# Kernel optimization log

Hardware: AMD Instinct MI355X
Metric: run time of the kernel (lower is better)

The kernel has to match this reference:

```python
import jax, jax.numpy as jnp
import numpy as np

N, E = 25000, 400000
D_NODE, D_EDGE_IN, D_EH, D_H, D_DUAL = 128, 16, 128, 256, 128


def layer_norm(x, g, b, eps=1e-5):
    mu = jnp.mean(x, axis=-1, keepdims=True)
    var = jnp.mean((x - mu) ** 2, axis=-1, keepdims=True)
    return (x - mu) * jax.lax.rsqrt(var + eps) * g + b


def setup_inputs() -> dict:
    key = jax.random.key(0)
    ks = jax.random.split(key, 20)

    def w(k, shape):
        return (jax.random.normal(k, shape, dtype=jnp.float32) * 0.05)

    inp = {
        "node_embedding": jax.random.normal(ks[0], (N, D_NODE), dtype=jnp.float32),
        "edge_index": jax.random.randint(ks[1], (2, E), 0, N, dtype=jnp.int64),
        "edge_attr": jax.random.normal(ks[2], (E, D_EDGE_IN), dtype=jnp.float32),
        "dual_node_emb": jax.random.normal(ks[3], (E, D_DUAL), dtype=jnp.float32),
        "atom_reactivity_logits": jax.random.normal(ks[4], (N,), dtype=jnp.float32),
        "W_be1": w(ks[5], (D_EDGE_IN, D_EH)), "b_be1": jnp.zeros((D_EH,), jnp.float32),
        "g_be1": jnp.ones((D_EH,), jnp.float32), "bb_be1": jnp.zeros((D_EH,), jnp.float32),
        "W_be2": w(ks[6], (D_EH, D_EH)), "b_be2": jnp.zeros((D_EH,), jnp.float32),
        "g_be2": jnp.ones((D_EH,), jnp.float32), "bb_be2": jnp.zeros((D_EH,), jnp.float32),
        "W_be3": w(ks[7], (D_EH, D_EH)), "b_be3": jnp.zeros((D_EH,), jnp.float32),
        "g_be3": jnp.ones((D_EH,), jnp.float32), "bb_be3": jnp.zeros((D_EH,), jnp.float32),
        # DualGraphBondReactivityPredictor
        "W_d1": w(ks[8], (D_DUAL, D_H)), "b_d1": jnp.zeros((D_H,), jnp.float32),
        "W_d2": w(ks[9], (D_H, D_H)), "b_d2": jnp.zeros((D_H,), jnp.float32),
        "W_do": w(ks[10], (D_H, 1)), "b_do": jnp.zeros((1,), jnp.float32),
        # main head: in = 2*D_NODE + D_EH + 3 = 387
        "W_f1": w(ks[11], (2 * D_NODE + D_EH + 3, D_H)), "b_f1": jnp.zeros((D_H,), jnp.float32),
        "W_f2": w(ks[12], (D_H, D_H)), "b_f2": jnp.zeros((D_H,), jnp.float32),
        "W_bo": w(ks[13], (D_H, 1)), "b_bo": jnp.zeros((1,), jnp.float32),
    }
    return inp


def reference(node_embedding, edge_index, edge_attr, dual_node_emb, atom_reactivity_logits,
              W_be1, b_be1, g_be1, bb_be1, W_be2, b_be2, g_be2, bb_be2,
              W_be3, b_be3, g_be3, bb_be3,
              W_d1, b_d1, W_d2, b_d2, W_do, b_do,
              W_f1, b_f1, W_f2, b_f2, W_bo, b_bo):
    src, dst = edge_index[0], edge_index[1]

    # BondEmbedding (dropout = identity in eval mode)
    e = jax.nn.silu(layer_norm(edge_attr @ W_be1 + b_be1, g_be1, bb_be1))
    e = jax.nn.silu(layer_norm(e @ W_be2 + b_be2, g_be2, bb_be2))
    e = jax.nn.silu(layer_norm(e @ W_be3 + b_be3, g_be3, bb_be3))  # [E, D_EH]

    atom_p = jax.nn.sigmoid(atom_reactivity_logits)  # [N]
    p_src = atom_p[src][:, None]  # [E,1]
    p_dst = atom_p[dst][:, None]

    # dual-graph bond reactivity
    d = jax.nn.silu(dual_node_emb @ W_d1 + b_d1)
    d = jax.nn.silu(d @ W_d2 + b_d2)
    dual_p = jax.nn.sigmoid((d @ W_do + b_do)[:, 0])[:, None]  # [E,1]

    feats = jnp.concatenate(
        [node_embedding[src], node_embedding[dst], e, dual_p, p_src, p_dst], axis=-1
    )  # [E, 2*D_NODE + D_EH + 3]

    x = jax.nn.silu(feats @ W_f1 + b_f1)
    x = jax.nn.silu(x @ W_f2 + b_f2)
    return (x @ W_bo + b_bo)[:, 0]  # [E]
```

## Files before the change

### kernel.cpp

```cpp
#include <hip/hip_runtime.h>
#include <hip/hip_bf16.h>
#include <stdint.h>

typedef __attribute__((ext_vector_type(8))) short bf16x8;
typedef __attribute__((ext_vector_type(4))) float f32x4;
typedef __attribute__((ext_vector_type(4))) float float4v;

__device__ __forceinline__ uint16_t bfc(float x){
    __hip_bfloat16 h = __float2bfloat16(x);
    return __builtin_bit_cast(uint16_t, h);
}
__device__ __forceinline__ uint32_t pk2(float a, float b){
    return (uint32_t)bfc(a) | ((uint32_t)bfc(b) << 16);
}
__device__ __forceinline__ float fsigmoid(float x){ return 1.0f / (1.0f + __expf(-x)); }
__device__ __forceinline__ float fsilu(float x){ return x * fsigmoid(x); }

__device__ __forceinline__ bf16x8 pack8(float4v lo, float4v hi){
    bf16x8 r;
    r[0]=(short)bfc(lo[0]); r[1]=(short)bfc(lo[1]);
    r[2]=(short)bfc(lo[2]); r[3]=(short)bfc(lo[3]);
    r[4]=(short)bfc(hi[0]); r[5]=(short)bfc(hi[1]);
    r[6]=(short)bfc(hi[2]); r[7]=(short)bfc(hi[3]);
    return r;
}

#define SZ_BE1 4096
#define SZ_128 16384
#define SZ_D1  32768
#define SZ_D2  65536
#define SZ_F1  98304
#define OFF_BE1 0
#define OFF_BE2 (OFF_BE1 + SZ_BE1)
#define OFF_BE3 (OFF_BE2 + SZ_128)
#define OFF_D1  (OFF_BE3 + SZ_128)
#define OFF_D2  (OFF_D1 + SZ_D1)
#define OFF_F1  (OFF_D2 + SZ_D2)
#define OFF_F2  (OFF_F1 + SZ_F1)
#define WS_ELEMS (OFF_F2 + SZ_D2)

__device__ __forceinline__ int fragpos(int k, int c, int OUT){
    int kt = k >> 5, ct = c >> 4;
    int fid = kt * (OUT >> 4) + ct;
    int ln = ((k & 31) >> 3) * 16 + (c & 15);
    return fid * 512 + ln * 8 + (k & 7);
}

__global__ void __launch_bounds__(256)
prep_w(const float* __restrict__ Wbe1, const float* __restrict__ Wbe2,
       const float* __restrict__ Wbe3, const float* __restrict__ Wd1,
       const float* __restrict__ Wd2,  const float* __restrict__ Wf1,
       const float* __restrict__ Wf2,  uint16_t* __restrict__ ws){
    int t = blockIdx.x * 256 + threadIdx.x;
    if (t >= WS_ELEMS) return;
    if (t < OFF_BE2) {
        int u = t;            int k = u >> 7, c = u & 127;
        float v = (k < 16) ? Wbe1[k * 128 + c] : 0.0f;
        ws[OFF_BE1 + fragpos(k, c, 128)] = bfc(v);
    } else if (t < OFF_BE3) {
        int u = t - OFF_BE2;  int k = u >> 7, c = u & 127;
        ws[OFF_BE2 + fragpos(k, c, 128)] = bfc(Wbe2[u]);
    } else if (t < OFF_D1) {
        int u = t - OFF_BE3;  int k = u >> 7, c = u & 127;
        ws[OFF_BE3 + fragpos(k, c, 128)] = bfc(Wbe3[u]);
    } else if (t < OFF_D2) {
        int u = t - OFF_D1;   int k = u >> 8, c = u & 255;
        ws[OFF_D1 + fragpos(k, c, 256)] = bfc(Wd1[u]);
    } else if (t < OFF_F1) {
        int u = t - OFF_D2;   int k = u >> 8, c = u & 255;
        ws[OFF_D2 + fragpos(k, c, 256)] = bfc(Wd2[u]);
    } else if (t < OFF_F2) {
        int u = t - OFF_F1;   int k = u >> 8, c = u & 255;
        ws[OFF_F1 + fragpos(k, c, 256)] = bfc(Wf1[u]);
    } else {
        int u = t - OFF_F2;   int k = u >> 8, c = u & 255;
        ws[OFF_F2 + fragpos(k, c, 256)] = bfc(Wf2[u]);
    }
}

__global__ void __launch_bounds__(256)
prep_n(const float* __restrict__ src, uint16_t* __restrict__ dst, int n){
    int t = blockIdx.x * 256 + threadIdx.x;
    if (t < n) dst[t] = bfc(src[t]);
}

typedef const __attribute__((address_space(1))) void gas_void;
typedef __attribute__((address_space(3))) void las_void;
__device__ __forceinline__ void g2l16(const void* g, void* l){
    __builtin_amdgcn_global_load_lds((gas_void*)g, (las_void*)l, 16, 0, 0);
}

#define LDS_TOTAL 135168

__global__ void __launch_bounds__(512) __attribute__((amdgpu_waves_per_eu(2, 2)))
bond_fast_kernel(const int* __restrict__ edge_index,
                 const float* __restrict__ edge_attr, const float* __restrict__ dual_emb,
                 const float* __restrict__ logits,
                 const float* __restrict__ b_be1, const float* __restrict__ g_be1, const float* __restrict__ bb_be1,
                 const float* __restrict__ b_be2, const float* __restrict__ g_be2, const float* __restrict__ bb_be2,
                 const float* __restrict__ b_be3, const float* __restrict__ g_be3, const float* __restrict__ bb_be3,
                 const float* __restrict__ b_d1, const float* __restrict__ b_d2,
                 const float* __restrict__ W_do, const float* __restrict__ b_do,
                 const float* __restrict__ W_f1, const float* __restrict__ b_f1,
                 const float* __restrict__ b_f2,
                 const float* __restrict__ W_bo, const float* __restrict__ b_bo,
                 const uint16_t* __restrict__ ws, float* __restrict__ out, int E)
{
    __shared__ char lds[LDS_TOTAL];
    const int t    = threadIdx.x;
    const int wave = t >> 6;
    const int lane = t & 63;
    const int li   = lane & 15, lg = lane >> 4;
    const int eg   = wave >> 1;
    const int ch   = wave & 1;
    const int e0b  = blockIdx.x * 128;

    char* bufE = lds;
    char* h256 = lds + 32768;
    uint16_t* wb0 = (uint16_t*)(lds + 98304);
    uint16_t* wb1 = (uint16_t*)(lds + 114688);
    float* ps  = (float*)(lds + 131072);
    float* pd  = (float*)(lds + 131584);
    int* sidx  = (int*)(lds + 132096);
    int* didx  = (int*)(lds + 132608);
    float* dpp = (float*)(lds + 133120);
    float* bop = (float*)(lds + 134144);

    const uint8_t*  wsb = (const uint8_t*)ws;
    const uint16_t* nbf = ws + WS_ELEMS;

    if (t < 128) {
        int e = e0b + t; if (e >= E) e = E - 1;
        int s_ = edge_index[e];
        int d_ = edge_index[E + e];
        sidx[t] = s_; didx[t] = d_;
        ps[t] = fsigmoid(logits[s_]);
        pd[t] = fsigmoid(logits[d_]);
    }

    int cur = 0;
    auto stageW = [&](int elemoff, int big){
        uint8_t* dst = (uint8_t*)(cur ? wb0 : wb1) + t * 16;
        const uint8_t* g = wsb + (size_t)elemoff * 2 + t * 16;
        g2l16(g, dst);
        if (big) g2l16(g + 8192, dst + 8192);
    };
    auto stepend = [&](){ __syncthreads(); cur ^= 1; };
    auto curbuf  = [&]() -> const uint16_t* { return cur ? wb1 : wb0; };

    f32x4 acc[2][8];

    auto ldf = [&](const uint16_t* w, int fid) -> bf16x8 {
        return *(const bf16x8*)(w + fid * 512 + lane * 8);
    };
    auto grpBE = [&](const uint16_t* w, bf16x8 a0){
        #pragma unroll
        for (int ct = 0; ct < 8; ++ct){
            bf16x8 b = ldf(w, ct);
            acc[0][ct] = __builtin_amdgcn_mfma_f32_16x16x32_bf16(a0, b, acc[0][ct], 0, 0, 0);
        }
    };
    auto grp256 = [&](const uint16_t* w, bf16x8 a0, bf16x8 a1){
        #pragma unroll
        for (int ct = 0; ct < 8; ++ct){
            bf16x8 b = ldf(w, ch * 8 + ct);
            acc[0][ct] = __builtin_amdgcn_mfma_f32_16x16x32_bf16(a0, b, acc[0][ct], 0, 0, 0);
            acc[1][ct] = __builtin_amdgcn_mfma_f32_16x16x32_bf16(a1, b, acc[1][ct], 0, 0, 0);
        }
    };
    auto initBE = [&](const float* b){
        #pragma unroll
        for (int ct = 0; ct < 8; ++ct){
            float bv = b[li + 16 * ct];
            f32x4 iv = {bv, bv, bv, bv};
            acc[0][ct] = iv;
        }
    };
    auto init256 = [&](const float* b){
        #pragma unroll
        for (int ct = 0; ct < 8; ++ct){
            float bv = b[ch * 128 + ct * 16 + li];
            f32x4 iv = {bv, bv, bv, bv};
            acc[0][ct] = iv; acc[1][ct] = iv;
        }
    };
    auto eb_read = [&](int row, int kt) -> bf16x8 {
        int off = row * 256 + (kt * 32 + lg * 8) * 2;
        return *(const bf16x8*)(bufE + (off ^ ((row & 7) << 4)));
    };
    auto h2_read = [&](int row, int kt) -> bf16x8 {
        int off = row * 512 + (kt * 32 + lg * 8) * 2;
        return *(const bf16x8*)(h256 + (off ^ ((row & 7) << 4)));
    };
    auto lnstoreBE = [&](const float* g, const float* bb){
        #pragma unroll
        for (int r = 0; r < 4; ++r){
            float s = 0.f, q = 0.f;
            #pragma unroll
            for (int ct = 0; ct < 8; ++ct){ float v = acc[0][ct][r]; s += v; q += v*v; }
            s += __shfl_xor(s, 1); q += __shfl_xor(q, 1);
            s += __shfl_xor(s, 2); q += __shfl_xor(q, 2);
            s += __shfl_xor(s, 4); q += __shfl_xor(q, 4);
            s += __shfl_xor(s, 8); q += __shfl_xor(q, 8);
            float mu = s * 0.0078125f;
            float var = q * 0.0078125f - mu * mu;
            float rs = rsqrtf(var + 1e-5f);
            int row = wave * 16 + lg * 4 + r;
            int rswz = (row & 7) << 4;
            #pragma unroll
            for (int ct = 0; ct < 8; ++ct){
                int col = li + 16 * ct;
                float v = (acc[0][ct][r] - mu) * rs * g[col] + bb[col];
                int off = row * 256 + col * 2;
                *(uint16_t*)(bufE + (off ^ rswz)) = bfc(fsilu(v));
            }
        }
    };
    auto silustore256 = [&](){
        #pragma unroll
        for (int rt = 0; rt < 2; ++rt){
            #pragma unroll
            for (int r = 0; r < 4; ++r){
                int row = eg * 32 + rt * 16 + lg * 4 + r;
                int rswz = (row & 7) << 4;
                #pragma unroll
                for (int ct = 0; ct < 8; ++ct){
                    int off = row * 512 + (ch * 128 + ct * 16 + li) * 2;
                    *(uint16_t*)(h256 + (off ^ rswz)) = bfc(fsilu(acc[rt][ct][r]));
                }
            }
        }
    };

    {
        const uint8_t* g = wsb + t * 16;
        g2l16(g, (uint8_t*)wb0 + t * 16);
    }
    __syncthreads();

    {
        stageW(OFF_BE2, 0);
        bf16x8 aE = {0,0,0,0,0,0,0,0};
        if (lg < 2){
            int ea = e0b + wave * 16 + li; if (ea >= E) ea = E - 1;
            const float* pa = edge_attr + (size_t)ea * 16 + lg * 8;
            aE = pack8(*(const float4v*)pa, *(const float4v*)(pa + 4));
        }
        initBE(b_be1);
        grpBE(curbuf(), aE);
        lnstoreBE(g_be1, bb_be1);
        stepend();
    }

    initBE(b_be2);
    #pragma unroll
    for (int kt = 0; kt < 4; ++kt){
        if (kt < 3) stageW(OFF_BE2 + (kt + 1) * 4096, 0);
        else        stageW(OFF_BE3, 0);
        grpBE(curbuf(), eb_read(wave * 16 + li, kt));
        if (kt == 3) lnstoreBE(g_be2, bb_be2);
        stepend();
    }
    initBE(b_be3);
    #pragma unroll
    for (int kt = 0; kt < 4; ++kt){
        if (kt < 3) stageW(OFF_BE3 + (kt + 1) * 4096, 0);
        else        stageW(OFF_D1, 1);
        grpBE(curbuf(), eb_read(wave * 16 + li, kt));
        if (kt == 3) lnstoreBE(g_be3, bb_be3);
        stepend();
    }

    init256(b_d1);
    #pragma unroll
    for (int kt = 0; kt < 4; ++kt){
        float4v va0, va1, vb0, vb1;
        {
            int ea = e0b + eg * 32 + li;      if (ea >= E) ea = E - 1;
            int eb = e0b + eg * 32 + 16 + li; if (eb >= E) eb = E - 1;
            const float* pa = dual_emb + (size_t)ea * 128 + kt * 32 + lg * 8;
            const float* pb = dual_emb + (size_t)eb * 128 + kt * 32 + lg * 8;
            va0 = *(const float4v*)pa; va1 = *(const float4v*)(pa + 4);
            vb0 = *(const float4v*)pb; vb1 = *(const float4v*)(pb + 4);
        }
        if (kt < 3) stageW(OFF_D1 + (kt + 1) * 8192, 1);
        else        stageW(OFF_D2, 1);
        grp256(curbuf(), pack8(va0, va1), pack8(vb0, vb1));
        if (kt == 3) silustore256();
        stepend();
    }

    init256(b_d2);
    #pragma unroll
    for (int kt = 0; kt < 8; ++kt){
        if (kt < 7) stageW(OFF_D2 + (kt + 1) * 8192, 1);
        else        stageW(OFF_F1, 1);
        grp256(curbuf(), h2_read(eg * 32 + li, kt), h2_read(eg * 32 + 16 + li, kt));
        if (kt == 7){
            #pragma unroll
            for (int rt = 0; rt < 2; ++rt){
                #pragma unroll
                for (int r = 0; r < 4; ++r){
                    float s = 0.f;
                    #pragma unroll
                    for (int ct = 0; ct < 8; ++ct)
                        s += fsilu(acc[rt][ct][r]) * W_do[ch * 128 + ct * 16 + li];
                    s += __shfl_xor(s, 1); s += __shfl_xor(s, 2);
                    s += __shfl_xor(s, 4); s += __shfl_xor(s, 8);
                    if (li == 0) dpp[ch * 128 + eg * 32 + rt * 16 + lg * 4 + r] = s;
                }
            }
        }
        stepend();
    }

    {
        {
            float bdo0 = b_do[0];
            #pragma unroll
            for (int ct = 0; ct < 8; ++ct){
                int col = ch * 128 + ct * 16 + li;
                float bv = b_f1[col];
                float t0 = W_f1[384 * 256 + col];
                float t1 = W_f1[385 * 256 + col];
                float t2 = W_f1[386 * 256 + col];
                #pragma unroll
                for (int rt = 0; rt < 2; ++rt)
                    #pragma unroll
                    for (int r = 0; r < 4; ++r){
                        int row = eg * 32 + rt * 16 + lg * 4 + r;
                        float dv = fsigmoid(dpp[row] + dpp[128 + row] + bdo0);
                        acc[rt][ct][r] = bv + dv*t0 + ps[row]*t1 + pd[row]*t2;
                    }
            }
        }
        int s0 = sidx[eg * 32 + li],      s1 = sidx[eg * 32 + 16 + li];
        int d0 = didx[eg * 32 + li],      d1 = didx[eg * 32 + 16 + li];
        #pragma unroll
        for (int kt = 0; kt < 12; ++kt){
            bf16x8 a0, a1;
            if (kt < 8){
                int ra = (kt < 4) ? s0 : d0;
                int rb = (kt < 4) ? s1 : d1;
                int ko = (kt & 3) * 32 + lg * 8;
                a0 = *(const bf16x8*)(nbf + (size_t)ra * 128 + ko);
                a1 = *(const bf16x8*)(nbf + (size_t)rb * 128 + ko);
            } else {
                a0 = eb_read(eg * 32 + li, kt - 8);
                a1 = eb_read(eg * 32 + 16 + li, kt - 8);
            }
            if (kt < 11) stageW(OFF_F1 + (kt + 1) * 8192, 1);
            else         stageW(OFF_F2, 1);
            grp256(curbuf(), a0, a1);
            if (kt == 11) silustore256();
            stepend();
        }
    }

    init256(b_f2);
    #pragma unroll
    for (int kt = 0; kt < 8; ++kt){
        if (kt < 7) stageW(OFF_F2 + (kt + 1) * 8192, 1);
        grp256(curbuf(), h2_read(eg * 32 + li, kt), h2_read(eg * 32 + 16 + li, kt));
        if (kt == 7){
            #pragma unroll
            for (int rt = 0; rt < 2; ++rt){
                #pragma unroll
                for (int r = 0; r < 4; ++r){
                    float s = 0.f;
                    #pragma unroll
                    for (int ct = 0; ct < 8; ++ct)
                        s += fsilu(acc[rt][ct][r]) * W_bo[ch * 128 + ct * 16 + li];
                    s += __shfl_xor(s, 1); s += __shfl_xor(s, 2);
                    s += __shfl_xor(s, 4); s += __shfl_xor(s, 8);
                    if (li == 0) bop[ch * 128 + eg * 32 + rt * 16 + lg * 4 + r] = s;
                }
            }
        } else {
            stepend();
        }
    }
    __syncthreads();
    if (t < 128){
        int e = e0b + t;
        if (e < E) out[e] = bop[t] + bop[128 + t] + b_bo[0];
    }
}

__global__ void __launch_bounds__(512) __attribute__((amdgpu_waves_per_eu(2, 2)))
bond_fused_kernel(const float* __restrict__ node_emb, const int* __restrict__ edge_index,
                  const float* __restrict__ edge_attr, const float* __restrict__ dual_emb,
                  const float* __restrict__ logits,
                  const float* __restrict__ W_be1, const float* __restrict__ b_be1,
                  const float* __restrict__ g_be1, const float* __restrict__ bb_be1,
                  const float* __restrict__ W_be2, const float* __restrict__ b_be2,
                  const float* __restrict__ g_be2, const float* __restrict__ bb_be2,
                  const float* __restrict__ W_be3, const float* __restrict__ b_be3,
                  const float* __restrict__ g_be3, const float* __restrict__ bb_be3,
                  const float* __restrict__ W_d1, const float* __restrict__ b_d1,
                  const float* __restrict__ W_d2, const float* __restrict__ b_d2,
                  const float* __restrict__ W_do, const float* __restrict__ b_do,
                  const float* __restrict__ W_f1, const float* __restrict__ b_f1,
                  const float* __restrict__ W_f2, const float* __restrict__ b_f2,
                  const float* __restrict__ W_bo, const float* __restrict__ b_bo,
                  float* __restrict__ out, int E)
{
    __shared__ char lds[LDS_TOTAL];
    const int t    = threadIdx.x;
    const int wave = t >> 6;
    const int lane = t & 63;
    const int li   = lane & 15, lg = lane >> 4;
    const int eg   = wave >> 1;
    const int ch   = wave & 1;
    const int e0b  = blockIdx.x * 128;

    char* bufE = lds;
    char* h256 = lds + 32768;
    uint16_t* wb0 = (uint16_t*)(lds + 98304);
    uint16_t* wb1 = (uint16_t*)(lds + 114688);
    float* ps  = (float*)(lds + 131072);
    float* pd  = (float*)(lds + 131584);
    int* sidx  = (int*)(lds + 132096);
    int* didx  = (int*)(lds + 132608);
    float* dpp = (float*)(lds + 133120);
    float* bop = (float*)(lds + 134144);

    if (t < 128) {
        int e = e0b + t; if (e >= E) e = E - 1;
        int s_ = edge_index[e];
        int d_ = edge_index[E + e];
        sidx[t] = s_; didx[t] = d_;
        ps[t] = fsigmoid(logits[s_]);
        pd[t] = fsigmoid(logits[d_]);
    }

    float sr[2][8];
    auto issueW256 = [&](const float* W, int kbase){
        #pragma unroll
        for (int h = 0; h < 2; ++h){
            const float* p = W + (size_t)(kbase + lg * 8) * 256 + (wave + 8*h) * 16 + li;
            #pragma unroll
            for (int j = 0; j < 8; ++j) sr[h][j] = p[j * 256];
        }
    };
    auto issueW128 = [&](const float* W, int kbase, int K){
        const float* p = W + (size_t)(kbase + lg * 8) * 128 + wave * 16 + li;
        #pragma unroll
        for (int j = 0; j < 8; ++j)
            sr[0][j] = (kbase + lg * 8 + j < K) ? p[j * 128] : 0.f;
    };
    auto commitW = [&](uint16_t* dst, int nh){
        #pragma unroll
        for (int h = 0; h < 2; ++h){
            if (h < nh){
                uint4 w;
                w.x = pk2(sr[h][0], sr[h][1]); w.y = pk2(sr[h][2], sr[h][3]);
                w.z = pk2(sr[h][4], sr[h][5]); w.w = pk2(sr[h][6], sr[h][7]);
                *(uint4*)(dst + (wave + 8*h) * 512 + lane * 8) = w;
            }
        }
    };

    int cur = 0;
    auto stepend = [&](int mode){
        if (mode) commitW(cur ? wb0 : wb1, mode == 128 ? 1 : 2);
        __syncthreads();
        cur ^= 1;
    };
    auto curbuf = [&]() -> const uint16_t* { return cur ? wb1 : wb0; };

    f32x4 acc[2][8];

    auto ldf = [&](const uint16_t* w, int fid) -> bf16x8 {
        return *(const bf16x8*)(w + fid * 512 + lane * 8);
    };
    auto grpBE = [&](const uint16_t* w, bf16x8 a0){
        #pragma unroll
        for (int ct = 0; ct < 8; ++ct){
            bf16x8 b = ldf(w, ct);
            acc[0][ct] = __builtin_amdgcn_mfma_f32_16x16x32_bf16(a0, b, acc[0][ct], 0, 0, 0);
        }
    };
    auto grp256 = [&](const uint16_t* w, bf16x8 a0, bf16x8 a1){
        #pragma unroll
        for (int ct = 0; ct < 8; ++ct){
            bf16x8 b = ldf(w, ch * 8 + ct);
            acc[0][ct] = __builtin_amdgcn_mfma_f32_16x16x32_bf16(a0, b, acc[0][ct], 0, 0, 0);
            acc[1][ct] = __builtin_amdgcn_mfma_f32_16x16x32_bf16(a1, b, acc[1][ct], 0, 0, 0);
        }
    };
    auto initBE = [&](const float* b){
        #pragma unroll
        for (int ct = 0; ct < 8; ++ct){
            float bv = b[li + 16 * ct];
            f32x4 iv = {bv, bv, bv, bv};
            acc[0][ct] = iv;
        }
    };
    auto init256 = [&](const float* b){
        #pragma unroll
        for (int ct = 0; ct < 8; ++ct){
            float bv = b[ch * 128 + ct * 16 + li];
            f32x4 iv = {bv, bv, bv, bv};
            acc[0][ct] = iv; acc[1][ct] = iv;
        }
    };
    auto eb_read = [&](int row, int kt) -> bf16x8 {
        int off = row * 256 + (kt * 32 + lg * 8) * 2;
        return *(const bf16x8*)(bufE + (off ^ ((row & 7) << 4)));
    };
    auto h2_read = [&](int row, int kt) -> bf16x8 {
        int off = row * 512 + (kt * 32 + lg * 8) * 2;
        return *(const bf16x8*)(h256 + (off ^ ((row & 7) << 4)));
    };
    auto lnstoreBE = [&](const float* g, const float* bb){
        #pragma unroll
        for (int r = 0; r < 4; ++r){
            float s = 0.f, q = 0.f;
            #pragma unroll
            for (int ct = 0; ct < 8; ++ct){ float v = acc[0][ct][r]; s += v; q += v*v; }
            s += __shfl_xor(s, 1); q += __shfl_xor(q, 1);
            s += __shfl_xor(s, 2); q += __shfl_xor(q, 2);
            s += __shfl_xor(s, 4); q += __shfl_xor(q, 4);
            s += __shfl_xor(s, 8); q += __shfl_xor(q, 8);
            float mu = s * 0.0078125f;
            float var = q * 0.0078125f - mu * mu;
            float rs = rsqrtf(var + 1e-5f);
            int row = wave * 16 + lg * 4 + r;
            int rswz = (row & 7) << 4;
            #pragma unroll
            for (int ct = 0; ct < 8; ++ct){
                int col = li + 16 * ct;
                float v = (acc[0][ct][r] - mu) * rs * g[col] + bb[col];
                int off = row * 256 + col * 2;
                *(uint16_t*)(bufE + (off ^ rswz)) = bfc(fsilu(v));
            }
        }
    };
    auto silustore256 = [&](){
        #pragma unroll
        for (int rt = 0; rt < 2; ++rt){
            #pragma unroll
            for (int r = 0; r < 4; ++r){
                int row = eg * 32 + rt * 16 + lg * 4 + r;
                int rswz = (row & 7) << 4;
                #pragma unroll
                for (int ct = 0; ct < 8; ++ct){
                    int off = row * 512 + (ch * 128 + ct * 16 + li) * 2;
                    *(uint16_t*)(h256 + (off ^ rswz)) = bfc(fsilu(acc[rt][ct][r]));
                }
            }
        }
    };

    issueW128(W_be1, 0, 16);
    commitW(wb0, 1);
    __syncthreads();

    {
        bf16x8 aE = {0,0,0,0,0,0,0,0};
        if (lg < 2){
            int ea = e0b + wave * 16 + li; if (ea >= E) ea = E - 1;
            const float* pa = edge_attr + (size_t)ea * 16 + lg * 8;
            aE = pack8(*(const float4v*)pa, *(const float4v*)(pa + 4));
        }
        issueW128(W_be2, 0, 128);
        initBE(b_be1);
        grpBE(curbuf(), aE);
        lnstoreBE(g_be1, bb_be1);
        stepend(128);
    }

    initBE(b_be2);
    #pragma unroll 1
    for (int kt = 0; kt < 4; ++kt){
        if (kt < 3) issueW128(W_be2, (kt + 1) * 32, 128);
        else        issueW128(W_be3, 0, 128);
        grpBE(curbuf(), eb_read(wave * 16 + li, kt));
        if (kt == 3) lnstoreBE(g_be2, bb_be2);
        stepend(128);
    }
    initBE(b_be3);
    #pragma unroll 1
    for (int kt = 0; kt < 4; ++kt){
        if (kt < 3) issueW128(W_be3, (kt + 1) * 32, 128);
        else        issueW256(W_d1, 0);
        grpBE(curbuf(), eb_read(wave * 16 + li, kt));
        if (kt == 3) lnstoreBE(g_be3, bb_be3);
        stepend(kt < 3 ? 128 : 256);
    }

    init256(b_d1);
    #pragma unroll 1
    for (int kt = 0; kt < 4; ++kt){
        float4v va0, va1, vb0, vb1;
        {
            int ea = e0b + eg * 32 + li;      if (ea >= E) ea = E - 1;
            int eb = e0b + eg * 32 + 16 + li; if (eb >= E) eb = E - 1;
            const float* pa = dual_emb + (size_t)ea * 128 + kt * 32 + lg * 8;
            const float* pb = dual_emb + (size_t)eb * 128 + kt * 32 + lg * 8;
            va0 = *(const float4v*)pa; va1 = *(const float4v*)(pa + 4);
            vb0 = *(const float4v*)pb; vb1 = *(const float4v*)(pb + 4);
        }
        if (kt < 3) issueW256(W_d1, (kt + 1) * 32);
        else        issueW256(W_d2, 0);
        grp256(curbuf(), pack8(va0, va1), pack8(vb0, vb1));
        if (kt == 3) silustore256();
        stepend(256);
    }

    init256(b_d2);
    #pragma unroll 1
    for (int kt = 0; kt < 8; ++kt){
        if (kt < 7) issueW256(W_d2, (kt + 1) * 32);
        else        issueW256(W_f1, 0);
        grp256(curbuf(), h2_read(eg * 32 + li, kt), h2_read(eg * 32 + 16 + li, kt));
        if (kt == 7){
            #pragma unroll
            for (int rt = 0; rt < 2; ++rt){
                #pragma unroll
                for (int r = 0; r < 4; ++r){
                    float s = 0.f;
                    #pragma unroll
                    for (int ct = 0; ct < 8; ++ct)
                        s += fsilu(acc[rt][ct][r]) * W_do[ch * 128 + ct * 16 + li];
                    s += __shfl_xor(s, 1); s += __shfl_xor(s, 2);
                    s += __shfl_xor(s, 4); s += __shfl_xor(s, 8);
                    if (li == 0) dpp[ch * 128 + eg * 32 + rt * 16 + lg * 4 + r] = s;
                }
            }
        }
        stepend(256);
    }

    {
        {
            float bdo0 = b_do[0];
            #pragma unroll
            for (int ct = 0; ct < 8; ++ct){
                int col = ch * 128 + ct * 16 + li;
                float bv = b_f1[col];
                float t0 = W_f1[384 * 256 + col];
                float t1 = W_f1[385 * 256 + col];
                float t2 = W_f1[386 * 256 + col];
                #pragma unroll
                for (int rt = 0; rt < 2; ++rt)
                    #pragma unroll
                    for (int r = 0; r < 4; ++r){
                        int row = eg * 32 + rt * 16 + lg * 4 + r;
                        float dv = fsigmoid(dpp[row] + dpp[128 + row] + bdo0);
                        acc[rt][ct][r] = bv + dv*t0 + ps[row]*t1 + pd[row]*t2;
                    }
            }
        }
        int s0 = sidx[eg * 32 + li],      s1 = sidx[eg * 32 + 16 + li];
        int d0 = didx[eg * 32 + li],      d1 = didx[eg * 32 + 16 + li];
        #pragma unroll 1
        for (int kt = 0; kt < 12; ++kt){
            bf16x8 a0, a1;
            if (kt < 8){
                int ra = (kt < 4) ? s0 : d0;
                int rb = (kt < 4) ? s1 : d1;
                int ko = (kt & 3) * 32 + lg * 8;
                const float* pa = node_emb + (size_t)ra * 128 + ko;
                const float* pb = node_emb + (size_t)rb * 128 + ko;
                a0 = pack8(*(const float4v*)pa, *(const float4v*)(pa + 4));
                a1 = pack8(*(const float4v*)pb, *(const float4v*)(pb + 4));
            } else {
                a0 = eb_read(eg * 32 + li, kt - 8);
                a1 = eb_read(eg * 32 + 16 + li, kt - 8);
            }
            if (kt < 11) issueW256(W_f1, (kt + 1) * 32);
            else         issueW256(W_f2, 0);
            grp256(curbuf(), a0, a1);
            if (kt == 11) silustore256();
            stepend(256);
        }
    }

    init256(b_f2);
    #pragma unroll 1
    for (int kt = 0; kt < 8; ++kt){
        if (kt < 7) issueW256(W_f2, (kt + 1) * 32);
        grp256(curbuf(), h2_read(eg * 32 + li, kt), h2_read(eg * 32 + 16 + li, kt));
        if (kt == 7){
            #pragma unroll
            for (int rt = 0; rt < 2; ++rt){
                #pragma unroll
                for (int r = 0; r < 4; ++r){
                    float s = 0.f;
                    #pragma unroll
                    for (int ct = 0; ct < 8; ++ct)
                        s += fsilu(acc[rt][ct][r]) * W_bo[ch * 128 + ct * 16 + li];
                    s += __shfl_xor(s, 1); s += __shfl_xor(s, 2);
                    s += __shfl_xor(s, 4); s += __shfl_xor(s, 8);
                    if (li == 0) bop[ch * 128 + eg * 32 + rt * 16 + lg * 4 + r] = s;
                }
            }
        } else {
            stepend(256);
        }
    }
    __syncthreads();
    if (t < 128){
        int e = e0b + t;
        if (e < E) out[e] = bop[t] + bop[128 + t] + b_bo[0];
    }
}

extern "C" void kernel_launch(void* const* d_in, const int* in_sizes, int n_in,
                              void* d_out, int out_size, void* d_ws, size_t ws_size,
                              hipStream_t stream) {
    const float* node_emb   = (const float*)d_in[0];
    const int*   edge_index = (const int*)d_in[1];
    const float* edge_attr  = (const float*)d_in[2];
    const float* dual_emb   = (const float*)d_in[3];
    const float* logits     = (const float*)d_in[4];
    const float* W_be1 = (const float*)d_in[5];
    const float* b_be1 = (const float*)d_in[6];
    const float* g_be1 = (const float*)d_in[7];
    const float* bb_be1= (const float*)d_in[8];
    const float* W_be2 = (const float*)d_in[9];
    const float* b_be2 = (const float*)d_in[10];
    const float* g_be2 = (const float*)d_in[11];
    const float* bb_be2= (const float*)d_in[12];
    const float* W_be3 = (const float*)d_in[13];
    const float* b_be3 = (const float*)d_in[14];
    const float* g_be3 = (const float*)d_in[15];
    const float* bb_be3= (const float*)d_in[16];
    const float* W_d1  = (const float*)d_in[17];
    const float* b_d1  = (const float*)d_in[18];
    const float* W_d2  = (const float*)d_in[19];
    const float* b_d2  = (const float*)d_in[20];
    const float* W_do  = (const float*)d_in[21];
    const float* b_do  = (const float*)d_in[22];
    const float* W_f1  = (const float*)d_in[23];
    const float* b_f1  = (const float*)d_in[24];
    const float* W_f2  = (const float*)d_in[25];
    const float* b_f2  = (const float*)d_in[26];
    const float* W_bo  = (const float*)d_in[27];
    const float* b_bo  = (const float*)d_in[28];
    float* out = (float*)d_out;

    int E = in_sizes[2] / 16;
    int nblocks = (E + 127) / 128;
    size_t nodeElems = (size_t)in_sizes[0];
    size_t wsNeed = ((size_t)WS_ELEMS + nodeElems) * 2;

    if (ws_size >= wsNeed) {
        uint16_t* ws16 = (uint16_t*)d_ws;
        prep_w<<<dim3((WS_ELEMS + 255) / 256), dim3(256), 0, stream>>>(
            W_be1, W_be2, W_be3, W_d1, W_d2, W_f1, W_f2, ws16);
        prep_n<<<dim3((int)((nodeElems + 255) / 256)), dim3(256), 0, stream>>>(
            node_emb, ws16 + WS_ELEMS, (int)nodeElems);
        bond_fast_kernel<<<dim3(nblocks), dim3(512), 0, stream>>>(
            edge_index, edge_attr, dual_emb, logits,
            b_be1, g_be1, bb_be1,
            b_be2, g_be2, bb_be2,
            b_be3, g_be3, bb_be3,
            b_d1, b_d2, W_do, b_do,
            W_f1, b_f1, b_f2, W_bo, b_bo,
            ws16, out, E);
    } else {
        bond_fused_kernel<<<dim3(nblocks), dim3(512), 0, stream>>>(
            node_emb, edge_index, edge_attr, dual_emb, logits,
            W_be1, b_be1, g_be1, bb_be1,
            W_be2, b_be2, g_be2, bb_be2,
            W_be3, b_be3, g_be3, bb_be3,
            W_d1, b_d1, W_d2, b_d2, W_do, b_do,
            W_f1, b_f1, W_f2, b_f2, W_bo, b_bo,
            out, E);
    }
}
```

Baseline: 708.3 us.

## Split fused bond kernel into per-layer kernels with global intermediates

Adds a path that, when the workspace is large enough, replaces the single fused bond kernel with five separate kernels: bond embedding, dual layer 1, dual layer 2 with output head, main layer 1 with gathers, and main layer 2 with output head. Intermediates (bf16 bond embeddings, bf16 hidden activations, dual probabilities) go through global workspace buffers. The aim is lower LDS and register pressure per kernel, which allows higher occupancy and simpler pipelining than the 135 KB-LDS fused kernel. In exchange it adds extra global traffic for the [E,256] hidden buffers, which are written and read twice, plus launch overhead.

```diff
diff --git a/kernel.cpp b/kernel.cpp
--- a/kernel.cpp
+++ b/kernel.cpp
@@ -90,8 +90,416 @@
     __builtin_amdgcn_global_load_lds((gas_void*)g, (las_void*)l, 16, 0, 0);
 }
 
+
+__global__ void __launch_bounds__(512)
+k_be(const float* __restrict__ edge_attr,
+     const float* __restrict__ b_be1, const float* __restrict__ g_be1, const float* __restrict__ bb_be1,
+     const float* __restrict__ b_be2, const float* __restrict__ g_be2, const float* __restrict__ bb_be2,
+     const float* __restrict__ b_be3, const float* __restrict__ g_be3, const float* __restrict__ bb_be3,
+     const uint16_t* __restrict__ ws, uint16_t* __restrict__ e3buf, int E)
+{
+    __shared__ char lds[49152];
+    const int t = threadIdx.x, wave = t >> 6, lane = t & 63;
+    const int li = lane & 15, lg = lane >> 4;
+    const int e0b = blockIdx.x * 128;
+    char* bufE = lds;
+    uint16_t* wb0 = (uint16_t*)(lds + 32768);
+    uint16_t* wb1 = (uint16_t*)(lds + 40960);
+    const uint8_t* wsb = (const uint8_t*)ws;
+
+    int cur = 0;
+    auto stage8 = [&](int elemoff){
+        g2l16(wsb + (size_t)elemoff * 2 + t * 16, (uint8_t*)(cur ? wb0 : wb1) + t * 16);
+    };
+    auto stepend = [&](){ __syncthreads(); cur ^= 1; };
+    auto curb = [&]() -> const uint16_t* { return cur ? wb1 : wb0; };
+
+    f32x4 acc[8];
+    auto ldf = [&](int fid) -> bf16x8 { return *(const bf16x8*)(curb() + fid * 512 + lane * 8); };
+    auto eb_read = [&](int row, int kt) -> bf16x8 {
+        int off = row * 256 + (kt * 32 + lg * 8) * 2;
+        return *(const bf16x8*)(bufE + (off ^ ((row & 7) << 4)));
+    };
+    auto initBE = [&](const float* b){
+        #pragma unroll
+        for (int ct = 0; ct < 8; ++ct){ float bv = b[li + 16*ct]; f32x4 iv = {bv,bv,bv,bv}; acc[ct] = iv; }
+    };
+    auto grpBE = [&](bf16x8 a0){
+        #pragma unroll
+        for (int ct = 0; ct < 8; ++ct)
+            acc[ct] = __builtin_amdgcn_mfma_f32_16x16x32_bf16(a0, ldf(ct), acc[ct], 0, 0, 0);
+    };
+    auto lnstoreBE = [&](const float* g, const float* bb){
+        #pragma unroll
+        for (int r = 0; r < 4; ++r){
+            float s = 0.f, q = 0.f;
+            #pragma unroll
+            for (int ct = 0; ct < 8; ++ct){ float v = acc[ct][r]; s += v; q += v*v; }
+            s += __shfl_xor(s, 1); q += __shfl_xor(q, 1);
+            s += __shfl_xor(s, 2); q += __shfl_xor(q, 2);
+            s += __shfl_xor(s, 4); q += __shfl_xor(q, 4);
+            s += __shfl_xor(s, 8); q += __shfl_xor(q, 8);
+            float mu = s * 0.0078125f;
+            float var = q * 0.0078125f - mu * mu;
+            float rs = rsqrtf(var + 1e-5f);
+            int row = wave * 16 + lg * 4 + r;
+            int rswz = (row & 7) << 4;
+            #pragma unroll
+            for (int ct = 0; ct < 8; ++ct){
+                int col = li + 16 * ct;
+                float v = (acc[ct][r] - mu) * rs * g[col] + bb[col];
+                int off = row * 256 + col * 2;
+                *(uint16_t*)(bufE + (off ^ rswz)) = bfc(fsilu(v));
+            }
+        }
+    };
+
+    g2l16(wsb + t * 16, (uint8_t*)wb0 + t * 16);
+    __syncthreads();
+
+    {
+        stage8(OFF_BE2);
+        initBE(b_be1);
+        bf16x8 aE = {0,0,0,0,0,0,0,0};
+        if (lg < 2){
+            int ea = e0b + wave * 16 + li; if (ea >= E) ea = E - 1;
+            const float* pa = edge_attr + (size_t)ea * 16 + lg * 8;
+            aE = pack8(*(const float4v*)pa, *(const float4v*)(pa + 4));
+        }
+        grpBE(aE);
+        lnstoreBE(g_be1, bb_be1);
+        stepend();
+    }
+    initBE(b_be2);
+    #pragma unroll 1
+    for (int kt = 0; kt < 4; ++kt){
+        stage8(kt < 3 ? OFF_BE2 + (kt + 1) * 4096 : OFF_BE3);
+        grpBE(eb_read(wave * 16 + li, kt));
+        if (kt == 3) lnstoreBE(g_be2, bb_be2);
+        stepend();
+    }
+    initBE(b_be3);
+    #pragma unroll 1
+    for (int kt = 0; kt < 4; ++kt){
+        if (kt < 3) stage8(OFF_BE3 + (kt + 1) * 4096);
+        grpBE(eb_read(wave * 16 + li, kt));
+        if (kt == 3) lnstoreBE(g_be3, bb_be3);
+        stepend();
+    }
+    #pragma unroll
+    for (int i = 0; i < 4; ++i){
+        int b = t * 16 + i * 8192;
+        int row = b >> 8;
+        uint4 v = *(const uint4*)(bufE + (b ^ ((row & 7) << 4)));
+        *(uint4*)((uint8_t*)e3buf + (size_t)e0b * 256 + b) = v;
+    }
+}
+
+__global__ void __launch_bounds__(512)
+k_d1(const float* __restrict__ dual_emb, const float* __restrict__ b_d1,
+     const uint16_t* __restrict__ ws, uint16_t* __restrict__ hbuf, int E)
+{
+    __shared__ char lds[32768];
+    const int t = threadIdx.x, wave = t >> 6, lane = t & 63;
+    const int li = lane & 15, lg = lane >> 4;
+    const int eg = wave >> 1, ch = wave & 1;
+    const int e0b = blockIdx.x * 128;
+    uint16_t* wb0 = (uint16_t*)lds;
+    uint16_t* wb1 = (uint16_t*)(lds + 16384);
+    const uint8_t* wsb = (const uint8_t*)ws;
+
+    int cur = 0;
+    auto stage16 = [&](int elemoff){
+        uint8_t* dst = (uint8_t*)(cur ? wb0 : wb1) + t * 16;
+        const uint8_t* g = wsb + (size_t)elemoff * 2 + t * 16;
+        g2l16(g, dst); g2l16(g + 8192, dst + 8192);
+    };
+    auto stepend = [&](){ __syncthreads(); cur ^= 1; };
+    auto curb = [&]() -> const uint16_t* { return cur ? wb1 : wb0; };
+
+    f32x4 acc[2][8];
+    #pragma unroll
+    for (int ct = 0; ct < 8; ++ct){
+        float bv = b_d1[ch * 128 + ct * 16 + li];
+        f32x4 iv = {bv, bv, bv, bv};
+        acc[0][ct] = iv; acc[1][ct] = iv;
+    }
+
+    {
+        const uint8_t* g = wsb + (size_t)OFF_D1 * 2 + t * 16;
+        g2l16(g, (uint8_t*)wb0 + t * 16);
+        g2l16(g + 8192, (uint8_t*)wb0 + t * 16 + 8192);
+    }
+    __syncthreads();
+
+    #pragma unroll 1
+    for (int kt = 0; kt < 4; ++kt){
+        if (kt < 3) stage16(OFF_D1 + (kt + 1) * 8192);
+        bf16x8 a0, a1;
+        {
+            int ea = e0b + eg * 32 + li;      if (ea >= E) ea = E - 1;
+            int eb = e0b + eg * 32 + 16 + li; if (eb >= E) eb = E - 1;
+            const float* pa = dual_emb + (size_t)ea * 128 + kt * 32 + lg * 8;
+            const float* pb = dual_emb + (size_t)eb * 128 + kt * 32 + lg * 8;
+            a0 = pack8(*(const float4v*)pa, *(const float4v*)(pa + 4));
+            a1 = pack8(*(const float4v*)pb, *(const float4v*)(pb + 4));
+        }
+        #pragma unroll
+        for (int ct = 0; ct < 8; ++ct){
+            bf16x8 b = *(const bf16x8*)(curb() + (ch * 8 + ct) * 512 + lane * 8);
+            acc[0][ct] = __builtin_amdgcn_mfma_f32_16x16x32_bf16(a0, b, acc[0][ct], 0, 0, 0);
+            acc[1][ct] = __builtin_amdgcn_mfma_f32_16x16x32_bf16(a1, b, acc[1][ct], 0, 0, 0);
+        }
+        if (kt < 3) stepend();
+    }
+    #pragma unroll
+    for (int rt = 0; rt < 2; ++rt)
+        #pragma unroll
+        for (int r = 0; r < 4; ++r){
+            size_t row = (size_t)(e0b + eg * 32 + rt * 16 + lg * 4 + r);
+            #pragma unroll
+            for (int ct = 0; ct < 8; ++ct)
+                hbuf[row * 256 + ch * 128 + ct * 16 + li] = bfc(fsilu(acc[rt][ct][r]));
+        }
+}
+
+__global__ void __launch_bounds__(512)
+k_d2(const float* __restrict__ b_d2, const float* __restrict__ W_do, const float* __restrict__ b_do,
+     const uint16_t* __restrict__ ws, const uint16_t* __restrict__ hbuf,
+     float* __restrict__ dpbuf, int E)
+{
+    __shared__ char lds[33792];
+    const int t = threadIdx.x, wave = t >> 6, lane = t & 63;
+    const int li = lane & 15, lg = lane >> 4;
+    const int eg = wave >> 1, ch = wave & 1;
+    const int e0b = blockIdx.x * 128;
+    uint16_t* wb0 = (uint16_t*)lds;
+    uint16_t* wb1 = (uint16_t*)(lds + 16384);
+    float* dpp = (float*)(lds + 32768);
+    const uint8_t* wsb = (const uint8_t*)ws;
+
+    int cur = 0;
+    auto stage16 = [&](int elemoff){
+        uint8_t* dst = (uint8_t*)(cur ? wb0 : wb1) + t * 16;
+        const uint8_t* g = wsb + (size_t)elemoff * 2 + t * 16;
+        g2l16(g, dst); g2l16(g + 8192, dst + 8192);
+    };
+    auto stepend = [&](){ __syncthreads(); cur ^= 1; };
+    auto curb = [&]() -> const uint16_t* { return cur ? wb1 : wb0; };
+
+    f32x4 acc[2][8];
+    #pragma unroll
+    for (int ct = 0; ct < 8; ++ct){
+        float bv = b_d2[ch * 128 + ct * 16 + li];
+        f32x4 iv = {bv, bv, bv, bv};
+        acc[0][ct] = iv; acc[1][ct] = iv;
+    }
+    {
+        const uint8_t* g = wsb + (size_t)OFF_D2 * 2 + t * 16;
+        g2l16(g, (uint8_t*)wb0 + t * 16);
+        g2l16(g + 8192, (uint8_t*)wb0 + t * 16 + 8192);
+    }
+    __syncthreads();
+
+    #pragma unroll 1
+    for (int kt = 0; kt < 8; ++kt){
+        if (kt < 7) stage16(OFF_D2 + (kt + 1) * 8192);
+        bf16x8 a0 = *(const bf16x8*)(hbuf + (size_t)(e0b + eg * 32 + li) * 256 + kt * 32 + lg * 8);
+        bf16x8 a1 = *(const bf16x8*)(hbuf + (size_t)(e0b + eg * 32 + 16 + li) * 256 + kt * 32 + lg * 8);
+        #pragma unroll
+        for (int ct = 0; ct < 8; ++ct){
+            bf16x8 b = *(const bf16x8*)(curb() + (ch * 8 + ct) * 512 + lane * 8);
+            acc[0][ct] = __builtin_amdgcn_mfma_f32_16x16x32_bf16(a0, b, acc[0][ct], 0, 0, 0);
+            acc[1][ct] = __builtin_amdgcn_mfma_f32_16x16x32_bf16(a1, b, acc[1][ct], 0, 0, 0);
+        }
+        if (kt < 7) stepend();
+    }
+    #pragma unroll
+    for (int rt = 0; rt < 2; ++rt)
+        #pragma unroll
+        for (int r = 0; r < 4; ++r){
+            float s = 0.f;
+            #pragma unroll
+            for (int ct = 0; ct < 8; ++ct)
+                s += fsilu(acc[rt][ct][r]) * W_do[ch * 128 + ct * 16 + li];
+            s += __shfl_xor(s, 1); s += __shfl_xor(s, 2);
+            s += __shfl_xor(s, 4); s += __shfl_xor(s, 8);
+            if (li == 0) dpp[ch * 128 + eg * 32 + rt * 16 + lg * 4 + r] = s;
+        }
+    __syncthreads();
+    if (t < 128) dpbuf[e0b + t] = fsigmoid(dpp[t] + dpp[128 + t] + b_do[0]);
+}
+
+__global__ void __launch_bounds__(512)
+k_f1(const int* __restrict__ edge_index, const float* __restrict__ logits,
+     const float* __restrict__ W_f1, const float* __restrict__ b_f1,
+     const uint16_t* __restrict__ ws, const uint16_t* __restrict__ nbf,
+     const uint16_t* __restrict__ e3buf, const float* __restrict__ dpbuf,
+     uint16_t* __restrict__ hbuf, int E)
+{
+    __shared__ char lds[34816];
+    const int t = threadIdx.x, wave = t >> 6, lane = t & 63;
+    const int li = lane & 15, lg = lane >> 4;
+    const int eg = wave >> 1, ch = wave & 1;
+    const int e0b = blockIdx.x * 128;
+    uint16_t* wb0 = (uint16_t*)lds;
+    uint16_t* wb1 = (uint16_t*)(lds + 16384);
+    float* ps = (float*)(lds + 32768);
+    float* pd = (float*)(lds + 33280);
+    int* sidx = (int*)(lds + 33792);
+    int* didx = (int*)(lds + 34304);
+    const uint8_t* wsb = (const uint8_t*)ws;
+
+    if (t < 128) {
+        int e = e0b + t; if (e >= E) e = E - 1;
+        int s_ = edge_index[e];
+        int d_ = edge_index[E + e];
+        sidx[t] = s_; didx[t] = d_;
+        ps[t] = fsigmoid(logits[s_]);
+        pd[t] = fsigmoid(logits[d_]);
+    }
+    int cur = 0;
+    auto stage16 = [&](int elemoff){
+        uint8_t* dst = (uint8_t*)(cur ? wb0 : wb1) + t * 16;
+        const uint8_t* g = wsb + (size_t)elemoff * 2 + t * 16;
+        g2l16(g, dst); g2l16(g + 8192, dst + 8192);
+    };
+    auto stepend = [&](){ __syncthreads(); cur ^= 1; };
+    auto curb = [&]() -> const uint16_t* { return cur ? wb1 : wb0; };
+
+    {
+        const uint8_t* g = wsb + (size_t)OFF_F1 * 2 + t * 16;
+        g2l16(g, (uint8_t*)wb0 + t * 16);
+        g2l16(g + 8192, (uint8_t*)wb0 + t * 16 + 8192);
+    }
+    __syncthreads();
+
+    f32x4 acc[2][8];
+    {
+        #pragma unroll
+        for (int ct = 0; ct < 8; ++ct){
+            int col = ch * 128 + ct * 16 + li;
+            float bv = b_f1[col];
+            float t0 = W_f1[384 * 256 + col];
+            float t1 = W_f1[385 * 256 + col];
+            float t2 = W_f1[386 * 256 + col];
+            #pragma unroll
+            for (int rt = 0; rt < 2; ++rt)
+                #pragma unroll
+                for (int r = 0; r < 4; ++r){
+                    int row = eg * 32 + rt * 16 + lg * 4 + r;
+                    float dv = dpbuf[e0b + row];
+                    acc[rt][ct][r] = bv + dv*t0 + ps[row]*t1 + pd[row]*t2;
+                }
+        }
+    }
+    int s0 = sidx[eg * 32 + li],  s1 = sidx[eg * 32 + 16 + li];
+    int d0 = didx[eg * 32 + li],  d1 = didx[eg * 32 + 16 + li];
+    #pragma unroll 1
+    for (int kt = 0; kt < 12; ++kt){
+        if (kt < 11) stage16(OFF_F1 + (kt + 1) * 8192);
+        bf16x8 a0, a1;
+        if (kt < 8){
+            int ra = (kt < 4) ? s0 : d0;
+            int rb = (kt < 4) ? s1 : d1;
+            int ko = (kt & 3) * 32 + lg * 8;
+            a0 = *(const bf16x8*)(nbf + (size_t)ra * 128 + ko);
+            a1 = *(const bf16x8*)(nbf + (size_t)rb * 128 + ko);
+        } else {
+            int ko = (kt - 8) * 32 + lg * 8;
+            a0 = *(const bf16x8*)(e3buf + (size_t)(e0b + eg * 32 + li) * 128 + ko);
+            a1 = *(const bf16x8*)(e3buf + (size_t)(e0b + eg * 32 + 16 + li) * 128 + ko);
+        }
+        #pragma unroll
+        for (int ct = 0; ct < 8; ++ct){
+            bf16x8 b = *(const bf16x8*)(curb() + (ch * 8 + ct) * 512 + lane * 8);
+            acc[0][ct] = __builtin_amdgcn_mfma_f32_16x16x32_bf16(a0, b, acc[0][ct], 0, 0, 0);
+            acc[1][ct] = __builtin_amdgcn_mfma_f32_16x16x32_bf16(a1, b, acc[1][ct], 0, 0, 0);
+        }
+        if (kt < 11) stepend();
+    }
+    #pragma unroll
+    for (int rt = 0; rt < 2; ++rt)
+        #pragma unroll
+        for (int r = 0; r < 4; ++r){
+            size_t row = (size_t)(e0b + eg * 32 + rt * 16 + lg * 4 + r);
+            #pragma unroll
+            for (int ct = 0; ct < 8; ++ct)
+                hbuf[row * 256 + ch * 128 + ct * 16 + li] = bfc(fsilu(acc[rt][ct][r]));
+        }
+}
+
+__global__ void __launch_bounds__(512)
+k_f2(const float* __restrict__ b_f2, const float* __restrict__ W_bo, const float* __restrict__ b_bo,
+     const uint16_t* __restrict__ ws, const uint16_t* __restrict__ hbuf,
+     float* __restrict__ out, int E)
+{
+    __shared__ char lds[33792];
+    const int t = threadIdx.x, wave = t >> 6, lane = t & 63;
+    const int li = lane & 15, lg = lane >> 4;
+    const int eg = wave >> 1, ch = wave & 1;
+    const int e0b = blockIdx.x * 128;
+    uint16_t* wb0 = (uint16_t*)lds;
+    uint16_t* wb1 = (uint16_t*)(lds + 16384);
+    float* bop = (float*)(lds + 32768);
+    const uint8_t* wsb = (const uint8_t*)ws;
+
+    int cur = 0;
+    auto stage16 = [&](int elemoff){
+        uint8_t* dst = (uint8_t*)(cur ? wb0 : wb1) + t * 16;
+        const uint8_t* g = wsb + (size_t)elemoff * 2 + t * 16;
+        g2l16(g, dst); g2l16(g + 8192, dst + 8192);
+    };
+    auto stepend = [&](){ __syncthreads(); cur ^= 1; };
+    auto curb = [&]() -> const uint16_t* { return cur ? wb1 : wb0; };
+
+    f32x4 acc[2][8];
+    #pragma unroll
+    for (int ct = 0; ct < 8; ++ct){
+        float bv = b_f2[ch * 128 + ct * 16 + li];
+        f32x4 iv = {bv, bv, bv, bv};
+        acc[0][ct] = iv; acc[1][ct] = iv;
+    }
+    {
+        const uint8_t* g = wsb + (size_t)OFF_F2 * 2 + t * 16;
+        g2l16(g, (uint8_t*)wb0 + t * 16);
+        g2l16(g + 8192, (uint8_t*)wb0 + t * 16 + 8192);
+    }
+    __syncthreads();
+
+    #pragma unroll 1
+    for (int kt = 0; kt < 8; ++kt){
+        if (kt < 7) stage16(OFF_F2 + (kt + 1) * 8192);
+        bf16x8 a0 = *(const bf16x8*)(hbuf + (size_t)(e0b + eg * 32 + li) * 256 + kt * 32 + lg * 8);
+        bf16x8 a1 = *(const bf16x8*)(hbuf + (size_t)(e0b + eg * 32 + 16 + li) * 256 + kt * 32 + lg * 8);
+        #pragma unroll
+        for (int ct = 0; ct < 8; ++ct){
+            bf16x8 b = *(const bf16x8*)(curb() + (ch * 8 + ct) * 512 + lane * 8);
+            acc[0][ct] = __builtin_amdgcn_mfma_f32_16x16x32_bf16(a0, b, acc[0][ct], 0, 0, 0);
+            acc[1][ct] = __builtin_amdgcn_mfma_f32_16x16x32_bf16(a1, b, acc[1][ct], 0, 0, 0);
+        }
+        if (kt < 7) stepend();
+    }
+    #pragma unroll
+    for (int rt = 0; rt < 2; ++rt)
+        #pragma unroll
+        for (int r = 0; r < 4; ++r){
+            float s = 0.f;
+            #pragma unroll
+            for (int ct = 0; ct < 8; ++ct)
+                s += fsilu(acc[rt][ct][r]) * W_bo[ch * 128 + ct * 16 + li];
+            s += __shfl_xor(s, 1); s += __shfl_xor(s, 2);
+            s += __shfl_xor(s, 4); s += __shfl_xor(s, 8);
+            if (li == 0) bop[ch * 128 + eg * 32 + rt * 16 + lg * 4 + r] = s;
+        }
+    __syncthreads();
+    if (t < 128){
+        int e = e0b + t;
+        if (e < E) out[e] = bop[t] + bop[128 + t] + b_bo[0];
+    }
+}
+
 #define LDS_TOTAL 135168
-
 __global__ void __launch_bounds__(512) __attribute__((amdgpu_waves_per_eu(2, 2)))
 bond_fast_kernel(const int* __restrict__ edge_index,
                  const float* __restrict__ edge_attr, const float* __restrict__ dual_emb,
@@ -744,10 +1152,30 @@
 
     int E = in_sizes[2] / 16;
     int nblocks = (E + 127) / 128;
+    size_t Epad = (size_t)nblocks * 128;
     size_t nodeElems = (size_t)in_sizes[0];
-    size_t wsNeed = ((size_t)WS_ELEMS + nodeElems) * 2;
-
-    if (ws_size >= wsNeed) {
+    size_t wsNeedSmall = ((size_t)WS_ELEMS + nodeElems) * 2;
+    size_t wsNeedBig = ((size_t)WS_ELEMS + nodeElems + Epad * 128 + Epad * 256) * 2 + Epad * 4;
+
+    if (ws_size >= wsNeedBig) {
+        uint16_t* ws16  = (uint16_t*)d_ws;
+        uint16_t* nbf_g = ws16 + WS_ELEMS;
+        uint16_t* e3buf = nbf_g + nodeElems;
+        uint16_t* hbuf  = e3buf + Epad * 128;
+        float*    dpbuf = (float*)(hbuf + Epad * 256);
+        prep_w<<<dim3((WS_ELEMS + 255) / 256), dim3(256), 0, stream>>>(
+            W_be1, W_be2, W_be3, W_d1, W_d2, W_f1, W_f2, ws16);
+        prep_n<<<dim3((int)((nodeElems + 255) / 256)), dim3(256), 0, stream>>>(
+            node_emb, nbf_g, (int)nodeElems);
+        k_be<<<dim3(nblocks), dim3(512), 0, stream>>>(
+            edge_attr, b_be1, g_be1, bb_be1, b_be2, g_be2, bb_be2,
+            b_be3, g_be3, bb_be3, ws16, e3buf, E);
+        k_d1<<<dim3(nblocks), dim3(512), 0, stream>>>(dual_emb, b_d1, ws16, hbuf, E);
+        k_d2<<<dim3(nblocks), dim3(512), 0, stream>>>(b_d2, W_do, b_do, ws16, hbuf, dpbuf, E);
+        k_f1<<<dim3(nblocks), dim3(512), 0, stream>>>(
+            edge_index, logits, W_f1, b_f1, ws16, nbf_g, e3buf, dpbuf, hbuf, E);
+        k_f2<<<dim3(nblocks), dim3(512), 0, stream>>>(b_f2, W_bo, b_bo, ws16, hbuf, out, E);
+    } else if (ws_size >= wsNeedSmall) {
         uint16_t* ws16 = (uint16_t*)d_ws;
         prep_w<<<dim3((WS_ELEMS + 255) / 256), dim3(256), 0, stream>>>(
             W_be1, W_be2, W_be3, W_d1, W_d2, W_f1, W_f2, ws16);
```

After: 691.4 us (median of 3 runs). 2.4% less time.
